# Kernel tuning notes

Hardware: AMD Instinct MI355X
Metric: run time of the kernel (lower is better)

## Reference

```python
import jax, jax.numpy as jnp
import numpy as np

D_MODEL = 64
HEADS = 8
LEVELS = 5
POINTS = 4
DH = D_MODEL // HEADS
EPS = 1e-5


def _layernorm(x, g, b):
    m = x.mean(-1, keepdims=True)
    v = ((x - m) ** 2).mean(-1, keepdims=True)
    return (x - m) / jnp.sqrt(v + EPS) * g + b


def _bilinear_sample(v, lx, ly, Hl, Wl):
    # v: (B, heads, Hl, Wl, dh); lx, ly: (B, Nq, heads, P) normalized in ~[0,1]
    # matches F.grid_sample(align_corners=False, padding_mode='zeros')
    x = lx * Wl - 0.5
    y = ly * Hl - 0.5
    x0 = jnp.floor(x)
    y0 = jnp.floor(y)
    wx = x - x0
    wy = y - y0
    x0i = x0.astype(jnp.int32)
    y0i = y0.astype(jnp.int32)
    B, heads = v.shape[0], v.shape[1]
    bidx = jnp.arange(B)[:, None, None, None]
    hidx = jnp.arange(heads)[None, None, :, None]

    def gather(yi, xi):
        valid = (xi >= 0) & (xi < Wl) & (yi >= 0) & (yi < Hl)
        xc = jnp.clip(xi, 0, Wl - 1)
        yc = jnp.clip(yi, 0, Hl - 1)
        g = v[bidx, hidx, yc, xc]  # (B, Nq, heads, P, dh)
        return g * valid[..., None].astype(v.dtype)

    return (gather(y0i, x0i) * ((1 - wx) * (1 - wy))[..., None]
            + gather(y0i, x0i + 1) * (wx * (1 - wy))[..., None]
            + gather(y0i + 1, x0i) * ((1 - wx) * wy)[..., None]
            + gather(y0i + 1, x0i + 1) * (wx * wy)[..., None])


def setup_inputs() -> dict:
    key = jax.random.key(0)
    ks = jax.random.split(key, 24)
    B, NQ = 2, 20000
    ss = np.array([[184, 184], [92, 92], [46, 46], [23, 23], [12, 12]], dtype=np.int64)
    areas = ss[:, 0] * ss[:, 1]
    lsi = np.concatenate([[0], np.cumsum(areas)[:-1]]).astype(np.int64)
    LIN = int(areas.sum())  # 45109
    s = 0.02
    inp = {
        'q_feat': jax.random.normal(ks[0], (B, NQ, D_MODEL), jnp.float32),
        'dense_voxel_flatten': jax.random.normal(ks[1], (B, LIN, D_MODEL), jnp.float32),
        'reference_points': jax.random.uniform(ks[2], (B, NQ, 2), jnp.float32),
        'q_pos': jax.random.normal(ks[3], (B, NQ, D_MODEL), jnp.float32),
        'spatial_shapes': ss,
        'level_start_index': lsi,
        'Wv': jax.random.normal(ks[4], (D_MODEL, D_MODEL), jnp.float32) * s,
        'bv': jnp.zeros((D_MODEL,), jnp.float32),
        'Wo': jax.random.normal(ks[5], (D_MODEL, HEADS * LEVELS * POINTS * 2), jnp.float32) * s,
        'bo': jax.random.normal(ks[6], (HEADS * LEVELS * POINTS * 2,), jnp.float32),
        'Wa': jax.random.normal(ks[7], (D_MODEL, HEADS * LEVELS * POINTS), jnp.float32) * s,
        'ba': jnp.zeros((HEADS * LEVELS * POINTS,), jnp.float32),
        'Wout': jax.random.normal(ks[8], (D_MODEL, D_MODEL), jnp.float32) * s,
        'bout': jnp.zeros((D_MODEL,), jnp.float32),
        'g1': jnp.ones((D_MODEL,), jnp.float32),
        'b1': jnp.zeros((D_MODEL,), jnp.float32),
        'W1': jax.random.normal(ks[9], (D_MODEL, 1024), jnp.float32) * s,
        'bff1': jnp.zeros((1024,), jnp.float32),
        'W2': jax.random.normal(ks[10], (1024, D_MODEL), jnp.float32) * s,
        'bff2': jnp.zeros((D_MODEL,), jnp.float32),
        'g2': jnp.ones((D_MODEL,), jnp.float32),
        'b2': jnp.zeros((D_MODEL,), jnp.float32),
    }
    return inp


def reference(q_feat, dense_voxel_flatten, reference_points, q_pos,
              spatial_shapes, level_start_index,
              Wv, bv, Wo, bo, Wa, ba, Wout, bout,
              g1, b1, W1, bff1, W2, bff2, g2, b2):
    B, NQ, _ = q_feat.shape
    q = q_feat + q_pos  # with_pos_embed
    value = (dense_voxel_flatten @ Wv + bv).reshape(B, -1, HEADS, DH)
    off = (q @ Wo + bo).reshape(B, NQ, HEADS, LEVELS, POINTS, 2)
    aw = jax.nn.softmax((q @ Wa + ba).reshape(B, NQ, HEADS, LEVELS * POINTS), axis=-1)
    aw = aw.reshape(B, NQ, HEADS, LEVELS, POINTS)
    # offset normalizer is (W, H) per level
    ssn = np.asarray(spatial_shapes)
    normalizer = jnp.asarray(ssn[:, ::-1].copy(), q.dtype)  # (L, 2)
    loc = reference_points[:, :, None, None, None, :] + off / normalizer[None, None, None, :, None, :]
    out = jnp.zeros((B, NQ, HEADS, DH), q.dtype)
    for l in range(LEVELS):
        Hl, Wl = int(ssn[l, 0]), int(ssn[l, 1])
        st = int(np.asarray(level_start_index)[l])
        vl = value[:, st:st + Hl * Wl].reshape(B, Hl, Wl, HEADS, DH).transpose(0, 3, 1, 2, 4)
        sampled = _bilinear_sample(vl, loc[:, :, :, l, :, 0], loc[:, :, :, l, :, 1], Hl, Wl)
        out = out + jnp.einsum('bnhpd,bnhp->bnhd', sampled, aw[:, :, :, l])
    attn_out = out.reshape(B, NQ, D_MODEL) @ Wout + bout
    x = _layernorm(q_feat + attn_out, g1, b1)  # residual + norm1 (dropout=0)
    ffn = jax.nn.relu(x @ W1 + bff1) @ W2 + bff2
    return _layernorm(x + ffn, g2, b2)
```

## Files before the change

### kernel.cpp

```cpp
#include <hip/hip_runtime.h>
#include <hip/hip_bf16.h>

#define NB 2
#define NQ 20000
#define DM 64
#define NH 8
#define NL 5
#define NP 4
#define LIN 45109
#define FFN 1024

typedef __attribute__((ext_vector_type(8))) short short8;
typedef __attribute__((ext_vector_type(4))) float f32x4;

__device__ __forceinline__ float b2f(const __hip_bfloat16 h) { return __bfloat162float(h); }
__device__ __forceinline__ float lo16f(unsigned u) { return __uint_as_float(u << 16); }
__device__ __forceinline__ float hi16f(unsigned u) { return __uint_as_float(u & 0xffff0000u); }
__device__ __forceinline__ unsigned f2bf_bits(float x) {
    unsigned u = __float_as_uint(x);
    return (u + 0x7FFFu + ((u >> 16) & 1u)) >> 16;
}

__global__ void __launch_bounds__(256)
prep_kernel(const float* __restrict__ dvf,
            const float* __restrict__ Wv, const float* __restrict__ bv,
            const float* __restrict__ W1, const float* __restrict__ W2,
            const float* __restrict__ Wo, const float* __restrict__ Wa,
            const float* __restrict__ Wout,
            __hip_bfloat16* __restrict__ W1p, __hip_bfloat16* __restrict__ W2p,
            __hip_bfloat16* __restrict__ Woap, __hip_bfloat16* __restrict__ Woutp,
            __hip_bfloat16* __restrict__ valA, __hip_bfloat16* __restrict__ valB,
            __hip_bfloat16* __restrict__ pad_ptr,
            int rows) {
    __shared__ __align__(16) __hip_bfloat16 wvp[8][64][8];
    __shared__ __align__(16) __hip_bfloat16 ar[64][72];
    __shared__ __align__(16) float bvs[64];

    const int tid = threadIdx.x;
    const int bid = blockIdx.x;
    const int lane = tid & 63;
    const int w = tid >> 6;
    const int m16 = lane & 15, qd = lane >> 4;

    if (bid < 81) {
        const int t = bid * 256 + tid;
        const int m = m16;
        const int seg = t >> 6;
        if (seg < 128) {
            const int nt = seg >> 1, kc = seg & 1;
            const int n = nt * 16 + m, kb = kc * 32 + qd * 8;
            __hip_bfloat16* dst = W1p + ((size_t)seg * 64 + lane) * 8;
#pragma unroll
            for (int j = 0; j < 8; j++) dst[j] = __float2bfloat16(W1[(size_t)(kb + j) * FFN + n]);
        } else if (seg < 256) {
            const int sl = seg - 128;
            const int nt = sl >> 5, kc = sl & 31;
            const int n = nt * 16 + m, kb = kc * 32 + qd * 8;
            __hip_bfloat16* dst = W2p + ((size_t)sl * 64 + lane) * 8;
#pragma unroll
            for (int j = 0; j < 8; j++) dst[j] = __float2bfloat16(W2[(size_t)(kb + j) * DM + n]);
        } else if (seg < 316) {
            const int sl = seg - 256;
            const int nt = sl >> 1, kc = sl & 1;
            const int n = nt * 16 + m, kb = kc * 32 + qd * 8;
            __hip_bfloat16* dst = Woap + ((size_t)sl * 64 + lane) * 8;
#pragma unroll
            for (int j = 0; j < 8; j++) {
                const int k = kb + j;
                const float v = (n < 320) ? Wo[(size_t)k * 320 + n] : Wa[(size_t)k * 160 + (n - 320)];
                dst[j] = __float2bfloat16(v);
            }
        } else if (seg < 324) {
            const int sl = seg - 316;
            const int nt = sl >> 1, kc = sl & 1;
            const int n = nt * 16 + m, kb = kc * 32 + qd * 8;
            __hip_bfloat16* dst = Woutp + ((size_t)sl * 64 + lane) * 8;
#pragma unroll
            for (int j = 0; j < 8; j++) dst[j] = __float2bfloat16(Wout[(size_t)(kb + j) * DM + n]);
        }
        return;
    }
    if (bid == 81) {
        uint4* p = (uint4*)pad_ptr;
        for (int i = tid; i < 1536; i += 256) p[i] = (uint4){0u, 0u, 0u, 0u};
        return;
    }

    const int row0 = (bid - 82) * 64;

    for (int idx = tid; idx < 4096; idx += 256) {
        const int j = idx & 7;
        const int l = (idx >> 3) & 63;
        const int seg = idx >> 9;
        const int nt = seg >> 1, kc = seg & 1;
        const int n = nt * 16 + (l & 15);
        const int k = kc * 32 + (l >> 4) * 8 + j;
        wvp[seg][l][j] = __float2bfloat16(Wv[k * 64 + n]);
    }
    if (tid < 64) bvs[tid] = bv[tid];

    {
        const int r = w * 16 + m16;
        const int grow = row0 + r;
        const int c0 = qd * 16;
        __hip_bfloat16* dst = &ar[r][c0];
        if (grow < rows) {
            const float4* src = (const float4*)&dvf[(size_t)grow * DM + c0];
#pragma unroll
            for (int t = 0; t < 4; t++) {
                const float4 v = src[t];
                dst[t * 4 + 0] = __float2bfloat16(v.x);
                dst[t * 4 + 1] = __float2bfloat16(v.y);
                dst[t * 4 + 2] = __float2bfloat16(v.z);
                dst[t * 4 + 3] = __float2bfloat16(v.w);
            }
        } else {
#pragma unroll
            for (int t = 0; t < 16; t++) dst[t] = __float2bfloat16(0.f);
        }
    }
    __syncthreads();

    f32x4 acc[4];
#pragma unroll
    for (int mt = 0; mt < 4; mt++) acc[mt] = (f32x4){0.f, 0.f, 0.f, 0.f};
#pragma unroll
    for (int kc = 0; kc < 2; kc++) {
        const short8 b = *(const short8*)&ar[w * 16 + m16][kc * 32 + qd * 8];
#pragma unroll
        for (int mt = 0; mt < 4; mt++) {
            const short8 a = *(const short8*)&wvp[mt * 2 + kc][lane][0];
            acc[mt] = __builtin_amdgcn_mfma_f32_16x16x32_bf16(a, b, acc[mt], 0, 0, 0);
        }
    }

    {
        const int vg = row0 + w * 16 + m16;
        if (vg < rows) {
            const int vr = (vg < LIN) ? vg : vg - LIN;
            __hip_bfloat16* dst = (vg < LIN) ? valA : valB;
#pragma unroll
            for (int mt = 0; mt < 4; mt++) {
                const int c0 = mt * 16 + qd * 4;
                const float4 bv4 = *(const float4*)&bvs[c0];
                const float r0 = acc[mt][0] + bv4.x, r1 = acc[mt][1] + bv4.y;
                const float r2 = acc[mt][2] + bv4.z, r3 = acc[mt][3] + bv4.w;
                uint2 u;
                u.x = f2bf_bits(r0) | (f2bf_bits(r1) << 16);
                u.y = f2bf_bits(r2) | (f2bf_bits(r3) << 16);
                *(uint2*)&dst[((size_t)(c0 >> 3) * LIN + vr) * 8 + (c0 & 7)] = u;
            }
        }
    }
}

__global__ void __launch_bounds__(256, 8)
attn4_kernel(const float* __restrict__ q_feat,
             const float* __restrict__ ref_pts,
             const float* __restrict__ q_pos,
             const __hip_bfloat16* __restrict__ Woap,
             const float* __restrict__ bo, const float* __restrict__ ba,
             const __hip_bfloat16* __restrict__ Woutp, const float* __restrict__ bout,
             const float* __restrict__ g1, const float* __restrict__ b1,
             const __hip_bfloat16* __restrict__ valA,
             const __hip_bfloat16* __restrict__ valB,
             int qoff,
             float* __restrict__ xout) {
    __shared__ __align__(16) __hip_bfloat16 qb[16][72];
    __shared__ __align__(16) float offs[4][321];
    __shared__ __align__(16) float aws[4][161];
    __shared__ __align__(16) float refs[4][2];
    __shared__ __align__(16) int4  dsc[640];

    float (*xs4)[64] = (float(*)[64])offs;

    const int tid = threadIdx.x;
    const int lane = tid & 63;
    const int w = tid >> 6;
    const int m16 = lane & 15, qd = lane >> 4;
    const int q0 = qoff + blockIdx.x * 4;
    const int qi = q0 + w;

    const int sz[NL]  = {184, 92, 46, 23, 12};
    const int lsi[NL] = {0, 33856, 42320, 44436, 44965};

    const __hip_bfloat16* valp = (q0 >= NQ) ? valB : valA;

    const float qf = q_feat[(size_t)qi * DM + lane];
    const float qp = q_pos[(size_t)qi * DM + lane];
    qb[w][lane] = __float2bfloat16(qf + qp);
    for (int idx = tid; idx < 12 * 16; idx += 256)
        *(uint2*)&qb[4 + (idx >> 4)][(idx & 15) * 4] = (uint2){0u, 0u};
    if (tid < 8) refs[tid >> 1][tid & 1] = ref_pts[(size_t)(q0 + (tid >> 1)) * 2 + (tid & 1)];
    __syncthreads();

    {
        const short8 qa0 = *(const short8*)&qb[m16][qd * 8];
        const short8 qa1 = *(const short8*)&qb[m16][32 + qd * 8];
#pragma unroll
        for (int t = 0; t < 8; t++) {
            const int nt = w + t * 4;
            if (nt < 30) {
                const short8 b0 = *(const short8*)(Woap + ((size_t)(nt * 2 + 0) * 64 + lane) * 8);
                const short8 b1 = *(const short8*)(Woap + ((size_t)(nt * 2 + 1) * 64 + lane) * 8);
                f32x4 acc = {0.f, 0.f, 0.f, 0.f};
                acc = __builtin_amdgcn_mfma_f32_16x16x32_bf16(qa0, b0, acc, 0, 0, 0);
                acc = __builtin_amdgcn_mfma_f32_16x16x32_bf16(qa1, b1, acc, 0, 0, 0);
                if (qd == 0) {
                    const int n = nt * 16 + m16;
                    if (n < 320) {
                        const float bn = bo[n];
#pragma unroll
                        for (int r = 0; r < 4; r++) offs[r][n] = acc[r] + bn;
                    } else {
                        const float bn = ba[n - 320];
#pragma unroll
                        for (int r = 0; r < 4; r++) aws[r][n - 320] = acc[r] + bn;
                    }
                }
            }
        }
    }
    __syncthreads();

    {
        const int g = tid >> 3;
        const int q = g >> 3, h = g & 7;
        const int j = tid & 7;
        float* p = &aws[q][h * 20];
        const float v0 = p[j], v1 = p[j + 8];
        const float v2 = (j < 4) ? p[j + 16] : -1e30f;
        float mx = fmaxf(fmaxf(v0, v1), v2);
        mx = fmaxf(mx, __shfl_xor(mx, 1, 8));
        mx = fmaxf(mx, __shfl_xor(mx, 2, 8));
        mx = fmaxf(mx, __shfl_xor(mx, 4, 8));
        const float e0 = __expf(v0 - mx), e1 = __expf(v1 - mx);
        const float e2 = (j < 4) ? __expf(v2 - mx) : 0.f;
        float s = e0 + e1 + e2;
        s += __shfl_xor(s, 1, 8);
        s += __shfl_xor(s, 2, 8);
        s += __shfl_xor(s, 4, 8);
        const float inv = 1.f / s;
        p[j] = e0 * inv;
        p[j + 8] = e1 * inv;
        if (j < 4) p[j + 16] = e2 * inv;
    }
    __syncthreads();

    for (int s = tid; s < 640; s += 256) {
        const int h = s & 7;
        const int t2 = s >> 3;
        const int p = t2 & 3;
        const int t3 = t2 >> 2;
        const int l = t3 % 5;
        const int q = t3 / 5;
        const int Wl = sz[l];
        const float Wf = (float)Wl;
        const int st = lsi[l];
        const int c = ((h * 5 + l) * 4 + p) * 2;
        const float fx = fmaf(refs[q][0], Wf, offs[q][c]) - 0.5f;
        const float fy = fmaf(refs[q][1], Wf, offs[q][c + 1]) - 0.5f;
        const float x0f = floorf(fx), y0f = floorf(fy);
        const float wx = fx - x0f, wy = fy - y0f;
        const int x0 = (int)x0f, y0 = (int)y0f;
        const float aV = aws[q][h * 20 + l * 4 + p];
        const bool xin0 = (x0 >= 0) & (x0 < Wl);
        const bool xin1 = (x0 >= -1) & (x0 < Wl - 1);
        const bool yin0 = (y0 >= 0) & (y0 < Wl);
        const bool yin1 = (y0 >= -1) & (y0 < Wl - 1);
        const float w00 = (xin0 & yin0) ? (1.f - wx) * (1.f - wy) * aV : 0.f;
        const float w10 = (xin1 & yin0) ? wx * (1.f - wy) * aV : 0.f;
        const float w01 = (xin0 & yin1) ? (1.f - wx) * wy * aV : 0.f;
        const float w11 = (xin1 & yin1) ? wx * wy * aV : 0.f;
        int b0 = (st + y0 * Wl + x0) * 8;
        b0 = b0 < -1520 ? -1520 : b0;
        b0 = b0 > LIN * 8 ? LIN * 8 : b0;
        const int b1i = b0 + Wl * 8;
        int4 d4;
        d4.x = b0;
        d4.y = b1i;
        d4.z = (int)(f2bf_bits(w00) | (f2bf_bits(w10) << 16));
        d4.w = (int)(f2bf_bits(w01) | (f2bf_bits(w11) << 16));
        dsc[s] = d4;
    }
    __syncthreads();

    {
        const int h = lane >> 3, j = lane & 7;
        const int c = j & 3;
        const int sp = j >> 2;
        const __hip_bfloat16* vbase = valp + (size_t)h * (LIN * 8) + (c & 1) * 8;
        float acc[8] = {0.f, 0.f, 0.f, 0.f, 0.f, 0.f, 0.f, 0.f};
#pragma unroll
        for (int g = 0; g < 2; g++) {
            short8 v[5];
            unsigned wb[5];
#pragma unroll
            for (int k = 0; k < 5; k++) {
                const int s = 2 * (g * 5 + k) + sp;
                const int4 d4 = dsc[(w * 20 + s) * 8 + h];
                const int base = (c >= 2) ? d4.y : d4.x;
                wb[k] = (unsigned)((c >= 2) ? d4.w : d4.z);
                v[k] = *(const short8*)(vbase + base);
            }
#pragma unroll
            for (int k = 0; k < 5; k++) {
                const float wt = (c & 1) ? hi16f(wb[k]) : lo16f(wb[k]);
#pragma unroll
                for (int d = 0; d < 8; d++)
                    acc[d] = fmaf(wt, __uint_as_float(((unsigned)(unsigned short)v[k][d]) << 16), acc[d]);
            }
        }
        const bool hi4 = (j & 4) != 0;
        float k4[4], gv4[4];
#pragma unroll
        for (int d = 0; d < 4; d++) {
            k4[d] = hi4 ? acc[d + 4] : acc[d];
            gv4[d] = hi4 ? acc[d] : acc[d + 4];
        }
#pragma unroll
        for (int d = 0; d < 4; d++) k4[d] += __shfl_xor(gv4[d], 4, 64);
        const bool hi2 = (j & 2) != 0;
        float k2[2], gv2[2];
#pragma unroll
        for (int d = 0; d < 2; d++) {
            k2[d] = hi2 ? k4[d + 2] : k4[d];
            gv2[d] = hi2 ? k4[d] : k4[d + 2];
        }
#pragma unroll
        for (int d = 0; d < 2; d++) k2[d] += __shfl_xor(gv2[d], 2, 64);
        const bool hi1 = (j & 1) != 0;
        float k1 = hi1 ? k2[1] : k2[0];
        float gv1 = hi1 ? k2[0] : k2[1];
        k1 += __shfl_xor(gv1, 1, 64);
        qb[w][lane] = __float2bfloat16(k1);
    }
    __syncthreads();

    {
        f32x4 acc = {0.f, 0.f, 0.f, 0.f};
#pragma unroll
        for (int kc = 0; kc < 2; kc++) {
            const short8 a = *(const short8*)&qb[m16][kc * 32 + qd * 8];
            const short8 b = *(const short8*)(Woutp + ((size_t)(w * 2 + kc) * 64 + lane) * 8);
            acc = __builtin_amdgcn_mfma_f32_16x16x32_bf16(a, b, acc, 0, 0, 0);
        }
        if (qd == 0) {
            const int n = w * 16 + m16;
            const float bn = bout[n];
#pragma unroll
            for (int r = 0; r < 4; r++) xs4[r][n] = acc[r] + bn;
        }
    }
    __syncthreads();

    {
        const float xpre = qf + xs4[w][lane];
        float s = xpre, s2 = xpre * xpre;
#pragma unroll
        for (int o = 32; o >= 1; o >>= 1) {
            s += __shfl_xor(s, o, 64);
            s2 += __shfl_xor(s2, o, 64);
        }
        const float mean = s * (1.f / 64.f);
        const float var = s2 * (1.f / 64.f) - mean * mean;
        const float xn = (xpre - mean) * rsqrtf(var + 1e-5f);
        xout[(size_t)qi * DM + lane] = xn * g1[lane] + b1[lane];
    }
}

__global__ void __launch_bounds__(256)
ffn_kernel(const __hip_bfloat16* __restrict__ W1p, const float* __restrict__ bff1,
           const __hip_bfloat16* __restrict__ W2p, const float* __restrict__ bff2,
           const float* __restrict__ g2, const float* __restrict__ b2,
           float* __restrict__ io) {
    __shared__ __align__(16) __hip_bfloat16 xq[2][2][64][8];
    __shared__ __align__(16) __hip_bfloat16 hb[32][264];
    __shared__ __align__(16) float yr[32][64];

    const int tid = threadIdx.x;
    const int lane = tid & 63;
    const int w = tid >> 6;
    const int m16 = lane & 15, qd = lane >> 4;
    const int q0 = blockIdx.x * 32;

    {
        const int q = tid >> 3, i = tid & 7;
        const float4 v0 = *(const float4*)&io[(size_t)(q0 + q) * DM + i * 8];
        const float4 v1 = *(const float4*)&io[(size_t)(q0 + q) * DM + i * 8 + 4];
        uint2 ua, ub;
        ua.x = f2bf_bits(v0.x) | (f2bf_bits(v0.y) << 16);
        ua.y = f2bf_bits(v0.z) | (f2bf_bits(v0.w) << 16);
        ub.x = f2bf_bits(v1.x) | (f2bf_bits(v1.y) << 16);
        ub.y = f2bf_bits(v1.z) | (f2bf_bits(v1.w) << 16);
        uint4 u4 = {ua.x, ua.y, ub.x, ub.y};
        *(uint4*)&xq[q >> 4][i >> 2][(q & 15) + (i & 3) * 16][0] = u4;
    }
    __syncthreads();

    short8 bx[2][2];
#pragma unroll
    for (int nt = 0; nt < 2; nt++)
#pragma unroll
        for (int kc = 0; kc < 2; kc++)
            bx[nt][kc] = *(const short8*)&xq[nt][kc][lane][0];

    f32x4 yacc[2];
    yacc[0] = (f32x4){0.f, 0.f, 0.f, 0.f};
    yacc[1] = (f32x4){0.f, 0.f, 0.f, 0.f};

#pragma unroll
    for (int qtr = 0; qtr < 4; qtr++) {
#pragma unroll
        for (int mt = 0; mt < 4; mt++) {
            const int htl = mt * 4 + w;
            const int ht = qtr * 16 + htl;
            f32x4 acc[2];
            acc[0] = (f32x4){0.f, 0.f, 0.f, 0.f};
            acc[1] = (f32x4){0.f, 0.f, 0.f, 0.f};
#pragma unroll
            for (int kc = 0; kc < 2; kc++) {
                const short8 a = *(const short8*)(W1p + ((size_t)(ht * 2 + kc) * 64 + lane) * 8);
#pragma unroll
                for (int nt = 0; nt < 2; nt++)
                    acc[nt] = __builtin_amdgcn_mfma_f32_16x16x32_bf16(a, bx[nt][kc], acc[nt], 0, 0, 0);
            }
            const float4 b4 = *(const float4*)&bff1[ht * 16 + qd * 4];
#pragma unroll
            for (int nt = 0; nt < 2; nt++) {
                const float r0 = fmaxf(acc[nt][0] + b4.x, 0.f);
                const float r1 = fmaxf(acc[nt][1] + b4.y, 0.f);
                const float r2 = fmaxf(acc[nt][2] + b4.z, 0.f);
                const float r3 = fmaxf(acc[nt][3] + b4.w, 0.f);
                uint2 u;
                u.x = f2bf_bits(r0) | (f2bf_bits(r1) << 16);
                u.y = f2bf_bits(r2) | (f2bf_bits(r3) << 16);
                *(uint2*)&hb[nt * 16 + m16][htl * 16 + qd * 4] = u;
            }
        }
        __syncthreads();
#pragma unroll
        for (int kc2 = 0; kc2 < 8; kc2++) {
            const short8 b = *(const short8*)(W2p + ((size_t)(w * 32 + qtr * 8 + kc2) * 64 + lane) * 8);
#pragma unroll
            for (int mt = 0; mt < 2; mt++) {
                const short8 a = *(const short8*)&hb[mt * 16 + m16][kc2 * 32 + qd * 8];
                yacc[mt] = __builtin_amdgcn_mfma_f32_16x16x32_bf16(a, b, yacc[mt], 0, 0, 0);
            }
        }
        __syncthreads();
    }

    {
        const int n = w * 16 + m16;
        const float bn = bff2[n];
#pragma unroll
        for (int mt = 0; mt < 2; mt++)
#pragma unroll
            for (int r = 0; r < 4; r++) {
                const int mm = mt * 16 + qd * 4 + r;
                yr[mm][n] = yacc[mt][r] + bn;
            }
    }
    __syncthreads();

    {
        const int q = tid >> 3, i = tid & 7;
        const float4 x0 = *(const float4*)&io[(size_t)(q0 + q) * DM + i * 8];
        const float4 x1 = *(const float4*)&io[(size_t)(q0 + q) * DM + i * 8 + 4];
        float4 v0 = *(const float4*)&yr[q][i * 8];
        float4 v1 = *(const float4*)&yr[q][i * 8 + 4];
        v0.x += x0.x; v0.y += x0.y; v0.z += x0.z; v0.w += x0.w;
        v1.x += x1.x; v1.y += x1.y; v1.z += x1.z; v1.w += x1.w;
        float s = v0.x + v0.y + v0.z + v0.w + v1.x + v1.y + v1.z + v1.w;
        float s2 = v0.x * v0.x + v0.y * v0.y + v0.z * v0.z + v0.w * v0.w
                 + v1.x * v1.x + v1.y * v1.y + v1.z * v1.z + v1.w * v1.w;
#pragma unroll
        for (int o = 4; o >= 1; o >>= 1) { s += __shfl_xor(s, o, 64); s2 += __shfl_xor(s2, o, 64); }
        const float mean = s * (1.f / 64.f);
        const float var = s2 * (1.f / 64.f) - mean * mean;
        const float rstd = rsqrtf(var + 1e-5f);
        const float4 ga = *(const float4*)&g2[i * 8];
        const float4 gb = *(const float4*)&g2[i * 8 + 4];
        const float4 ba4 = *(const float4*)&b2[i * 8];
        const float4 bb4 = *(const float4*)&b2[i * 8 + 4];
        float4 o0, o1;
        o0.x = (v0.x - mean) * rstd * ga.x + ba4.x;
        o0.y = (v0.y - mean) * rstd * ga.y + ba4.y;
        o0.z = (v0.z - mean) * rstd * ga.z + ba4.z;
        o0.w = (v0.w - mean) * rstd * ga.w + ba4.w;
        o1.x = (v1.x - mean) * rstd * gb.x + bb4.x;
        o1.y = (v1.y - mean) * rstd * gb.y + bb4.y;
        o1.z = (v1.z - mean) * rstd * gb.z + bb4.z;
        o1.w = (v1.w - mean) * rstd * gb.w + bb4.w;
        *(float4*)&io[(size_t)(q0 + q) * DM + i * 8] = o0;
        *(float4*)&io[(size_t)(q0 + q) * DM + i * 8 + 4] = o1;
    }
}

extern "C" void kernel_launch(void* const* d_in, const int* in_sizes, int n_in,
                              void* d_out, int out_size, void* d_ws, size_t ws_size,
                              hipStream_t stream) {
    const int B0 = (in_sizes[4] >= 4096) ? 4 : 6;
    const float* q_feat = (const float*)d_in[0];
    const float* dvf    = (const float*)d_in[1];
    const float* refp   = (const float*)d_in[2];
    const float* q_pos  = (const float*)d_in[3];
    const float* Wv   = (const float*)d_in[B0 + 0];
    const float* bv   = (const float*)d_in[B0 + 1];
    const float* Wo   = (const float*)d_in[B0 + 2];
    const float* bo   = (const float*)d_in[B0 + 3];
    const float* Wa   = (const float*)d_in[B0 + 4];
    const float* ba   = (const float*)d_in[B0 + 5];
    const float* Wout = (const float*)d_in[B0 + 6];
    const float* bout = (const float*)d_in[B0 + 7];
    const float* g1   = (const float*)d_in[B0 + 8];
    const float* b1   = (const float*)d_in[B0 + 9];
    const float* W1   = (const float*)d_in[B0 + 10];
    const float* bff1 = (const float*)d_in[B0 + 11];
    const float* W2   = (const float*)d_in[B0 + 12];
    const float* bff2 = (const float*)d_in[B0 + 13];
    const float* g2   = (const float*)d_in[B0 + 14];
    const float* b2   = (const float*)d_in[B0 + 15];
    float* out = (float*)d_out;

    const size_t val_elems = (size_t)LIN * DM;
    const size_t pack_elems = (size_t)(128 + 128 + 60 + 8) * 64 * 8;
    const size_t PAD_ELEMS = 12288;
    const bool dbuf = ws_size >= (pack_elems + 2 * val_elems + PAD_ELEMS) * sizeof(__hip_bfloat16);

    __hip_bfloat16* W1p = (__hip_bfloat16*)d_ws;
    __hip_bfloat16* W2p = W1p + (size_t)128 * 64 * 8;
    __hip_bfloat16* Woap = W2p + (size_t)128 * 64 * 8;
    __hip_bfloat16* Woutp = Woap + (size_t)60 * 64 * 8;
    __hip_bfloat16* val0 = W1p + pack_elems;
    __hip_bfloat16* val1 = dbuf ? val0 + val_elems : val0;
    __hip_bfloat16* pad_ptr = val1 + val_elems;

    if (dbuf) {
        prep_kernel<<<82 + (2 * LIN + 63) / 64, 256, 0, stream>>>(
            dvf, Wv, bv, W1, W2, Wo, Wa, Wout,
            W1p, W2p, Woap, Woutp, val0, val1, pad_ptr, 2 * LIN);
        attn4_kernel<<<(NB * NQ) / 4, 256, 0, stream>>>(
            q_feat, refp, q_pos, Woap, bo, ba, Woutp, bout, g1, b1,
            val0, val1, 0, out);
    } else {
        for (int b = 0; b < NB; b++) {
            prep_kernel<<<82 + (LIN + 63) / 64, 256, 0, stream>>>(
                dvf + (size_t)b * val_elems, Wv, bv, W1, W2, Wo, Wa, Wout,
                W1p, W2p, Woap, Woutp, val0, val0, pad_ptr, LIN);
            attn4_kernel<<<NQ / 4, 256, 0, stream>>>(
                q_feat, refp, q_pos, Woap, bo, ba, Woutp, bout, g1, b1,
                val0, val0, b * NQ, out);
        }
    }
    ffn_kernel<<<(NB * NQ) / 32, 256, 0, stream>>>(W1p, bff1, W2p, bff2, g2, b2, out);
}
```

Baseline: 225.1 us.

## Fuse softmax with sampling descriptors and use packed FMA for bilinear gather

Folds the sampling-descriptor computation into the softmax stage, so each thread normalizes its attention weights in registers and writes descriptors directly. This removes one barrier and a round trip of normalized weights through shared memory. The zeroing of padded query rows is dropped, and the bf16-to-fp32 accumulate loop is rewritten with two-wide float vectors so the compiler can emit packed FMAs. An empty asm statement is added to force the gathered loads to complete before the FMAs. The descriptor index layout changes to (q*5+l)*32+p*8+h, which must match how the gather stage reads them. Leaving the pad rows unzeroed may feed garbage into the MFMA rows that are not stored.

Result: no change. 227.3 us (+1.0%).

```diff
diff --git a/kernel.cpp b/kernel.cpp
--- a/kernel.cpp
+++ b/kernel.cpp
@@ -12,6 +12,7 @@
 
 typedef __attribute__((ext_vector_type(8))) short short8;
 typedef __attribute__((ext_vector_type(4))) float f32x4;
+typedef __attribute__((ext_vector_type(2))) float f32x2;
 
 __device__ __forceinline__ float b2f(const __hip_bfloat16 h) { return __bfloat162float(h); }
 __device__ __forceinline__ float lo16f(unsigned u) { return __uint_as_float(u << 16); }
@@ -189,8 +190,6 @@
     const float qf = q_feat[(size_t)qi * DM + lane];
     const float qp = q_pos[(size_t)qi * DM + lane];
     qb[w][lane] = __float2bfloat16(qf + qp);
-    for (int idx = tid; idx < 12 * 16; idx += 256)
-        *(uint2*)&qb[4 + (idx >> 4)][(idx & 15) * 4] = (uint2){0u, 0u};
     if (tid < 8) refs[tid >> 1][tid & 1] = ref_pts[(size_t)(q0 + (tid >> 1)) * 2 + (tid & 1)];
     __syncthreads();
 
@@ -227,61 +226,55 @@
         const int g = tid >> 3;
         const int q = g >> 3, h = g & 7;
         const int j = tid & 7;
-        float* p = &aws[q][h * 20];
-        const float v0 = p[j], v1 = p[j + 8];
-        const float v2 = (j < 4) ? p[j + 16] : -1e30f;
+        const float* lg = &aws[q][h * 20];
+        const float v0 = lg[j], v1 = lg[j + 8];
+        const float v2 = (j < 4) ? lg[j + 16] : -1e30f;
         float mx = fmaxf(fmaxf(v0, v1), v2);
         mx = fmaxf(mx, __shfl_xor(mx, 1, 8));
         mx = fmaxf(mx, __shfl_xor(mx, 2, 8));
         mx = fmaxf(mx, __shfl_xor(mx, 4, 8));
         const float e0 = __expf(v0 - mx), e1 = __expf(v1 - mx);
         const float e2 = (j < 4) ? __expf(v2 - mx) : 0.f;
-        float s = e0 + e1 + e2;
-        s += __shfl_xor(s, 1, 8);
-        s += __shfl_xor(s, 2, 8);
-        s += __shfl_xor(s, 4, 8);
-        const float inv = 1.f / s;
-        p[j] = e0 * inv;
-        p[j + 8] = e1 * inv;
-        if (j < 4) p[j + 16] = e2 * inv;
-    }
-    __syncthreads();
-
-    for (int s = tid; s < 640; s += 256) {
-        const int h = s & 7;
-        const int t2 = s >> 3;
-        const int p = t2 & 3;
-        const int t3 = t2 >> 2;
-        const int l = t3 % 5;
-        const int q = t3 / 5;
-        const int Wl = sz[l];
-        const float Wf = (float)Wl;
-        const int st = lsi[l];
-        const int c = ((h * 5 + l) * 4 + p) * 2;
-        const float fx = fmaf(refs[q][0], Wf, offs[q][c]) - 0.5f;
-        const float fy = fmaf(refs[q][1], Wf, offs[q][c + 1]) - 0.5f;
-        const float x0f = floorf(fx), y0f = floorf(fy);
-        const float wx = fx - x0f, wy = fy - y0f;
-        const int x0 = (int)x0f, y0 = (int)y0f;
-        const float aV = aws[q][h * 20 + l * 4 + p];
-        const bool xin0 = (x0 >= 0) & (x0 < Wl);
-        const bool xin1 = (x0 >= -1) & (x0 < Wl - 1);
-        const bool yin0 = (y0 >= 0) & (y0 < Wl);
-        const bool yin1 = (y0 >= -1) & (y0 < Wl - 1);
-        const float w00 = (xin0 & yin0) ? (1.f - wx) * (1.f - wy) * aV : 0.f;
-        const float w10 = (xin1 & yin0) ? wx * (1.f - wy) * aV : 0.f;
-        const float w01 = (xin0 & yin1) ? (1.f - wx) * wy * aV : 0.f;
-        const float w11 = (xin1 & yin1) ? wx * wy * aV : 0.f;
-        int b0 = (st + y0 * Wl + x0) * 8;
-        b0 = b0 < -1520 ? -1520 : b0;
-        b0 = b0 > LIN * 8 ? LIN * 8 : b0;
-        const int b1i = b0 + Wl * 8;
-        int4 d4;
-        d4.x = b0;
-        d4.y = b1i;
-        d4.z = (int)(f2bf_bits(w00) | (f2bf_bits(w10) << 16));
-        d4.w = (int)(f2bf_bits(w01) | (f2bf_bits(w11) << 16));
-        dsc[s] = d4;
+        float ssum = e0 + e1 + e2;
+        ssum += __shfl_xor(ssum, 1, 8);
+        ssum += __shfl_xor(ssum, 2, 8);
+        ssum += __shfl_xor(ssum, 4, 8);
+        const float inv = 1.f / ssum;
+        const float rx = refs[q][0], ry = refs[q][1];
+
+        auto mkdesc = [&](int jp, float ev) {
+            const int l = jp >> 2, p = jp & 3;
+            const int Wl = sz[l];
+            const float Wf = (float)Wl;
+            const int st = lsi[l];
+            const int cc = ((h * 5 + l) * 4 + p) * 2;
+            const float fx = fmaf(rx, Wf, offs[q][cc]) - 0.5f;
+            const float fy = fmaf(ry, Wf, offs[q][cc + 1]) - 0.5f;
+            const float x0f = floorf(fx), y0f = floorf(fy);
+            const float wx = fx - x0f, wy = fy - y0f;
+            const int x0 = (int)x0f, y0 = (int)y0f;
+            const float aV = ev * inv;
+            const bool xin0 = (x0 >= 0) & (x0 < Wl);
+            const bool xin1 = (x0 >= -1) & (x0 < Wl - 1);
+            const bool yin0 = (y0 >= 0) & (y0 < Wl);
+            const bool yin1 = (y0 >= -1) & (y0 < Wl - 1);
+            const float w00 = (xin0 & yin0) ? (1.f - wx) * (1.f - wy) * aV : 0.f;
+            const float w10 = (xin1 & yin0) ? wx * (1.f - wy) * aV : 0.f;
+            const float w01 = (xin0 & yin1) ? (1.f - wx) * wy * aV : 0.f;
+            const float w11 = (xin1 & yin1) ? wx * wy * aV : 0.f;
+            int b0 = (st + y0 * Wl + x0) * 8;
+            b0 = b0 < -1520 ? -1520 : b0;
+            b0 = b0 > LIN * 8 ? LIN * 8 : b0;
+            int4 d4;
+            d4.x = b0;
+            d4.y = b0 + Wl * 8;
+            d4.z = (int)(f2bf_bits(w00) | (f2bf_bits(w10) << 16));
+            d4.w = (int)(f2bf_bits(w01) | (f2bf_bits(w11) << 16));
+            dsc[(q * 5 + l) * 32 + p * 8 + h] = d4;
+        };
+        mkdesc(j, e0);
+        mkdesc(j + 8, e1);
+        if (j < 4) mkdesc(j + 16, e2);
     }
     __syncthreads();
 
@@ -290,27 +283,41 @@
         const int c = j & 3;
         const int sp = j >> 2;
         const __hip_bfloat16* vbase = valp + (size_t)h * (LIN * 8) + (c & 1) * 8;
-        float acc[8] = {0.f, 0.f, 0.f, 0.f, 0.f, 0.f, 0.f, 0.f};
-#pragma unroll
-        for (int g = 0; g < 2; g++) {
-            short8 v[5];
-            unsigned wb[5];
+        f32x2 acc2[4];
+#pragma unroll
+        for (int d = 0; d < 4; d++) acc2[d] = (f32x2){0.f, 0.f};
+#pragma unroll
+        for (int gg = 0; gg < 2; gg++) {
+            short8 vv[5];
+            unsigned wbk[5];
 #pragma unroll
             for (int k = 0; k < 5; k++) {
-                const int s = 2 * (g * 5 + k) + sp;
+                const int s = 2 * (gg * 5 + k) + sp;
                 const int4 d4 = dsc[(w * 20 + s) * 8 + h];
                 const int base = (c >= 2) ? d4.y : d4.x;
-                wb[k] = (unsigned)((c >= 2) ? d4.w : d4.z);
-                v[k] = *(const short8*)(vbase + base);
-            }
+                wbk[k] = (unsigned)((c >= 2) ? d4.w : d4.z);
+                vv[k] = *(const short8*)(vbase + base);
+            }
+            asm volatile("" :: "v"(((const unsigned*)&vv[0])[0]),
+                              "v"(((const unsigned*)&vv[1])[0]),
+                              "v"(((const unsigned*)&vv[2])[0]),
+                              "v"(((const unsigned*)&vv[3])[0]),
+                              "v"(((const unsigned*)&vv[4])[0]));
 #pragma unroll
             for (int k = 0; k < 5; k++) {
-                const float wt = (c & 1) ? hi16f(wb[k]) : lo16f(wb[k]);
-#pragma unroll
-                for (int d = 0; d < 8; d++)
-                    acc[d] = fmaf(wt, __uint_as_float(((unsigned)(unsigned short)v[k][d]) << 16), acc[d]);
-            }
-        }
+                const float wt = (c & 1) ? hi16f(wbk[k]) : lo16f(wbk[k]);
+                const f32x2 wt2 = {wt, wt};
+#pragma unroll
+                for (int d = 0; d < 4; d++) {
+                    const unsigned u = ((const unsigned*)&vv[k])[d];
+                    const f32x2 val = {lo16f(u), hi16f(u)};
+                    acc2[d] = val * wt2 + acc2[d];
+                }
+            }
+        }
+        float acc[8];
+#pragma unroll
+        for (int d = 0; d < 4; d++) { acc[2 * d] = acc2[d][0]; acc[2 * d + 1] = acc2[d][1]; }
         const bool hi4 = (j & 4) != 0;
         float k4[4], gv4[4];
 #pragma unroll
```
